# Performance work log

Hardware: AMD Instinct MI355X
Metric: run time of the kernel (lower is better)

The kernel has to match this reference:

```python
import jax, jax.numpy as jnp
import numpy as np
from jax import lax

B, C, H, W = 8, 64, 128, 128
K = 3  # deformable kernel size, padding=1, stride=1


def conv3x3(x, w, b=None):
    # x: [B,Cin,H,W], w: [Cout,Cin,3,3]
    y = lax.conv_general_dilated(x, w, (1, 1), 'SAME',
                                 dimension_numbers=('NCHW', 'OIHW', 'NCHW'))
    if b is not None:
        y = y + b[None, :, None, None]
    return y


def leaky_relu(x, slope=0.1):
    return jnp.where(x >= 0, x, slope * x)


def _bilinear_sample_one(feat, ys, xs):
    # feat: [C,H,W]; ys, xs: [KK,H,W] fractional sample coords (zero outside borders)
    h, w = feat.shape[1], feat.shape[2]
    y0 = jnp.floor(ys)
    x0 = jnp.floor(xs)
    wy = ys - y0  # [KK,H,W]
    wx = xs - x0

    def gather(yi, xi):
        valid = ((yi >= 0) & (yi < h) & (xi >= 0) & (xi < w)).astype(feat.dtype)
        yc = jnp.clip(yi, 0, h - 1).astype(jnp.int32)
        xc = jnp.clip(xi, 0, w - 1).astype(jnp.int32)
        v = feat[:, yc, xc]  # [C,KK,H,W]
        return v * valid[None]

    v00 = gather(y0, x0)
    v01 = gather(y0, x0 + 1)
    v10 = gather(y0 + 1, x0)
    v11 = gather(y0 + 1, x0 + 1)
    top = v00 * (1 - wx)[None] + v01 * wx[None]
    bot = v10 * (1 - wx)[None] + v11 * wx[None]
    return top * (1 - wy)[None] + bot * wy[None]  # [C,KK,H,W]


def deform_conv2d(x, offset, weight):
    # x: [B,Cin,H,W]; offset: [B,2*K*K,H,W] (torchvision order: per-tap (dy,dx));
    # weight: [Cout,Cin,K,K]; stride=1, pad=1, dilation=1, groups=1, no bias.
    b, cin, h, w = x.shape
    kk = K * K
    off = offset.reshape(b, kk, 2, h, w)
    dy, dx = off[:, :, 0], off[:, :, 1]  # [B,KK,H,W]
    hh = jnp.arange(h, dtype=x.dtype)[:, None]
    ww = jnp.arange(w, dtype=x.dtype)[None, :]
    ky = (jnp.arange(kk) // K - 1).astype(x.dtype)[None, :, None, None]
    kx = (jnp.arange(kk) % K - 1).astype(x.dtype)[None, :, None, None]
    ys = hh[None, None] + ky + dy  # [B,KK,H,W]
    xs = ww[None, None] + kx + dx
    sampled = jax.vmap(_bilinear_sample_one)(x, ys, xs)  # [B,Cin,KK,H,W]
    wflat = weight.reshape(weight.shape[0], cin, kk)
    return jnp.einsum('bckhw,ock->bohw', sampled, wflat)


def setup_inputs() -> dict:
    key = jax.random.key(0)
    ks = jax.random.split(key, 7)
    ref_feat = jax.random.normal(ks[0], (B, C, H, W), jnp.float32)
    target_feat = jax.random.normal(ks[1], (B, C, H, W), jnp.float32)
    w1 = jax.random.normal(ks[2], (C, 2 * C, 3, 3), jnp.float32) * 0.02
    b1 = jax.random.normal(ks[3], (C,), jnp.float32) * 0.02
    w2 = jax.random.normal(ks[4], (18, C, 3, 3), jnp.float32) * 0.02
    b2 = jax.random.normal(ks[5], (18,), jnp.float32) * 0.02
    wd = jax.random.normal(ks[6], (C, C, 3, 3), jnp.float32) * 0.05
    return {'ref_feat': ref_feat, 'target_feat': target_feat,
            'w1': w1, 'b1': b1, 'w2': w2, 'b2': b2, 'wd': wd}


def reference(ref_feat, target_feat, w1, b1, w2, b2, wd):
    concat_feat = jnp.concatenate([ref_feat, target_feat], axis=1)  # [B,2C,H,W]
    hmid = leaky_relu(conv3x3(concat_feat, w1, b1), 0.1)
    offset = conv3x3(hmid, w2, b2)  # [B,18,H,W]
    aligned_feat = deform_conv2d(target_feat, offset, wd)  # [B,C,H,W]
    return aligned_feat
```

## Files before the change

### kernel.cpp

```cpp
#include <hip/hip_runtime.h>
#include <hip/hip_fp16.h>

#define HW 128
#define PLANE (HW * HW)
#define OSTR 22

typedef __attribute__((ext_vector_type(8))) _Float16 f16x8;
typedef __attribute__((ext_vector_type(4))) float f32x4;

__device__ __forceinline__ unsigned short f2h(float f) {
  return __half_as_ushort(__float2half(f));
}

__device__ __forceinline__ void tile_from_bid_512(int bid, int& b, int& by, int& bx) {
  int wg = (bid & 7) * 64 + (bid >> 3);
  b = wg >> 6;
  int t = wg & 63;
  by = (t >> 3) << 4;
  bx = (t & 7) << 4;
}

__global__ __launch_bounds__(256) void pack_all_kernel(
    const float* __restrict__ w1, const float* __restrict__ w2,
    const float* __restrict__ wd, unsigned short* __restrict__ w1p,
    unsigned short* __restrict__ w2p, unsigned short* __restrict__ wdp) {
  int idx = blockIdx.x * 256 + threadIdx.x;
  if (idx < 73728) {
    int k = idx >> 6, n = idx & 63;
    int tap = k >> 7, ic = k & 127;
    w1p[((k >> 3) * 64 + n) * 8 + (k & 7)] = f2h(w1[(n * 128 + ic) * 9 + tap]);
  } else if (idx < 73728 + 18432) {
    int i = idx - 73728;
    int k = i >> 5, n = i & 31;
    int tap = k >> 6, ic = k & 63;
    float v = (n < 18) ? w2[(n * 64 + ic) * 9 + tap] : 0.f;
    w2p[((k >> 3) * 32 + n) * 8 + (k & 7)] = f2h(v);
  } else if (idx < 73728 + 18432 + 36864) {
    int i = idx - 73728 - 18432;
    int k = i >> 6, n = i & 63;
    int tap = k >> 6, ic = k & 63;
    wdp[((k >> 3) * 64 + n) * 8 + (k & 7)] = f2h(wd[(n * 64 + ic) * 9 + tap]);
  }
}

__global__ __launch_bounds__(256) void to_nhwc_kernel(
    const float* __restrict__ ref, const float* __restrict__ tgt,
    unsigned short* __restrict__ xref, unsigned short* __restrict__ xtgt) {
  __shared__ unsigned short lds[32][136];
  const int b = blockIdx.z, y = blockIdx.y, x0 = blockIdx.x * 32;
  for (int idx = threadIdx.x; idx < 4096; idx += 256) {
    int ic = idx >> 5, px = idx & 31;
    const float* src = (ic < 64) ? ref : tgt;
    lds[px][ic] = f2h(src[(b * 64 + (ic & 63)) * PLANE + y * HW + x0 + px]);
  }
  __syncthreads();
  for (int idx = threadIdx.x; idx < 512; idx += 256) {
    int px = idx >> 4, g = idx & 15;
    uint4 v = *(const uint4*)&lds[px][g * 8];
    size_t base = ((size_t)(b * HW + y) * HW + x0 + px) * 64;
    if (g < 8)
      *(uint4*)(xref + base + g * 8) = v;
    else
      *(uint4*)(xtgt + base + (g - 8) * 8) = v;
  }
}

__device__ __forceinline__ uint4 blend4(uint4 a, uint4 b, uint4 c, uint4 d,
                                        __half2 h00, __half2 h01, __half2 h10, __half2 h11) {
  union U { uint4 u; __half2 h[4]; };
  U A, B, C, D, R;
  A.u = a; B.u = b; C.u = c; D.u = d;
#pragma unroll
  for (int i = 0; i < 4; ++i)
    R.h[i] = __hfma2(D.h[i], h11, __hfma2(C.h[i], h10, __hfma2(B.h[i], h01, __hmul2(A.h[i], h00))));
  return R.u;
}

__global__ __launch_bounds__(512, 2) void mega_kernel(
    const unsigned short* __restrict__ xref, const unsigned short* __restrict__ xtgt,
    const unsigned short* __restrict__ w1p, const float* __restrict__ b1,
    const unsigned short* __restrict__ w2p, const float* __restrict__ b2,
    const unsigned short* __restrict__ wdp, float* __restrict__ out) {
  __shared__ __align__(16) unsigned short bufW[400 * 64];
  __shared__ __align__(8) float offsL[256 * OSTR];

  int b, by, bx;
  tile_from_bid_512(blockIdx.x, b, by, bx);
  const int tid = threadIdx.x, lane = tid & 63, w = tid >> 6;
  const int l15 = lane & 15, lg = lane >> 4;

  const unsigned short* rb = xref + (size_t)b * PLANE * 64;
  const unsigned short* tb = xtgt + (size_t)b * PLANE * 64;

  auto STAGE = [&](const unsigned short* src) {
    for (int i = tid; i < 3200; i += 512) {
      int rec = i >> 3, g = i & 7;
      int wy = rec / 20, wx = rec - wy * 20;
      int gy = by - 2 + wy, gx = bx - 2 + wx;
      uint4 v = make_uint4(0u, 0u, 0u, 0u);
      if ((unsigned)gy < 128u && (unsigned)gx < 128u)
        v = *(const uint4*)(src + ((size_t)gy * HW + gx) * 64 + g * 8);
      *(uint4*)(bufW + rec * 64 + ((g * 8) ^ ((rec & 7) << 3))) = v;
    }
  };

  int pyv[3], pxv[3];
#pragma unroll
  for (int n = 0; n < 3; ++n) {
    int p = (w * 3 + n) * 16 + l15;
    p = min(p, 323);
    pyv[n] = p / 18;
    pxv[n] = p - pyv[n] * 18;
  }

  f32x4 acc1[4][3];
#pragma unroll
  for (int mf = 0; mf < 4; ++mf)
#pragma unroll
    for (int n = 0; n < 3; ++n) acc1[mf][n] = (f32x4){0.f, 0.f, 0.f, 0.f};

  auto CONV1_HALF = [&](int c) {
#pragma unroll
    for (int tap = 0; tap < 9; ++tap) {
      const int ty = tap / 3, tx = tap - ty * 3;
#pragma unroll
      for (int ks = 0; ks < 2; ++ks) {
        f16x8 bp[3];
#pragma unroll
        for (int n = 0; n < 3; ++n) {
          int rec = (pyv[n] + ty) * 20 + pxv[n] + tx;
          bp[n] = *(const f16x8*)(bufW + rec * 64 + ((ks * 32 + lg * 8) ^ ((rec & 7) << 3)));
        }
        const int kb = tap * 16 + c * 8 + ks * 4 + lg;
        f16x8 aw[4];
#pragma unroll
        for (int mf = 0; mf < 4; ++mf)
          aw[mf] = *(const f16x8*)(w1p + (kb * 64 + mf * 16 + l15) * 8);
#pragma unroll
        for (int mf = 0; mf < 4; ++mf)
#pragma unroll
          for (int n = 0; n < 3; ++n)
            acc1[mf][n] = __builtin_amdgcn_mfma_f32_16x16x32_f16(aw[mf], bp[n], acc1[mf][n], 0, 0, 0);
      }
    }
  };

  STAGE(tb);
  __syncthreads();
  CONV1_HALF(1);
  __syncthreads();
  STAGE(rb);
  __syncthreads();
  CONV1_HALF(0);
  __syncthreads();

  unsigned short* hmidL = bufW;
#pragma unroll
  for (int mf = 0; mf < 4; ++mf) {
    const float4 bv = ((const float4*)b1)[mf * 4 + lg];
#pragma unroll
    for (int n = 0; n < 3; ++n) {
      const int p = (w * 3 + n) * 16 + l15;
      const bool valid = ((unsigned)(by - 1 + pyv[n]) < 128u) &&
                         ((unsigned)(bx - 1 + pxv[n]) < 128u);
      const float m = valid ? 1.f : 0.f;
      float v0 = acc1[mf][n][0] + bv.x;
      float v1 = acc1[mf][n][1] + bv.y;
      float v2 = acc1[mf][n][2] + bv.z;
      float v3 = acc1[mf][n][3] + bv.w;
      v0 = ((v0 >= 0.f) ? v0 : 0.1f * v0) * m;
      v1 = ((v1 >= 0.f) ? v1 : 0.1f * v1) * m;
      v2 = ((v2 >= 0.f) ? v2 : 0.1f * v2) * m;
      v3 = ((v3 >= 0.f) ? v3 : 0.1f * v3) * m;
      ushort4 s;
      s.x = f2h(v0); s.y = f2h(v1); s.z = f2h(v2); s.w = f2h(v3);
      *(ushort4*)(hmidL + p * 64 + ((mf * 16 + lg * 4) ^ ((p & 7) << 3))) = s;
    }
  }
  __syncthreads();

  f32x4 acc2[2][2];
#pragma unroll
  for (int q = 0; q < 2; ++q)
#pragma unroll
    for (int nf = 0; nf < 2; ++nf) acc2[q][nf] = (f32x4){0.f, 0.f, 0.f, 0.f};

#pragma unroll
  for (int tap = 0; tap < 9; ++tap) {
    const int ty = tap / 3, tx = tap - ty * 3;
#pragma unroll
    for (int ks = 0; ks < 2; ++ks) {
      f16x8 ap[2];
#pragma unroll
      for (int q = 0; q < 2; ++q) {
        int p = (w * 2 + q + ty) * 18 + l15 + tx;
        ap[q] = *(const f16x8*)(hmidL + p * 64 + ((ks * 32 + lg * 8) ^ ((p & 7) << 3)));
      }
      const int kb = tap * 8 + ks * 4 + lg;
      f16x8 bw[2];
#pragma unroll
      for (int nf = 0; nf < 2; ++nf)
        bw[nf] = *(const f16x8*)(w2p + (kb * 32 + nf * 16 + l15) * 8);
#pragma unroll
      for (int q = 0; q < 2; ++q)
#pragma unroll
        for (int nf = 0; nf < 2; ++nf)
          acc2[q][nf] = __builtin_amdgcn_mfma_f32_16x16x32_f16(ap[q], bw[nf], acc2[q][nf], 0, 0, 0);
    }
  }
#pragma unroll
  for (int nf = 0; nf < 2; ++nf) {
    const int oc = nf * 16 + l15;
    if (oc < 18) {
      const float bias = b2[oc];
#pragma unroll
      for (int q = 0; q < 2; ++q)
#pragma unroll
        for (int reg = 0; reg < 4; ++reg) {
          int px = (w * 2 + q) * 16 + lg * 4 + reg;
          offsL[px * OSTR + oc] = acc2[q][nf][reg] + bias;
        }
    }
  }
  __syncthreads();

  STAGE(tb);
  __syncthreads();

  f32x4 acc[2][4];
#pragma unroll
  for (int q = 0; q < 2; ++q)
#pragma unroll
    for (int nf = 0; nf < 4; ++nf) acc[q][nf] = (f32x4){0.f, 0.f, 0.f, 0.f};

  const int x = bx + l15;

  for (int kk = 0; kk < 9; ++kk) {
    const int kdy = kk / 3 - 1, kdx = kk - (kk / 3) * 3 - 1;
    f16x8 af[2][2];
#pragma unroll
    for (int q = 0; q < 2; ++q) {
      const int y = by + w * 2 + q;
      const int px_lin = (w * 2 + q) * 16 + l15;
      const float2 o2 = *(const float2*)(&offsL[px_lin * OSTR + kk * 2]);
      float ys = (float)(y + kdy) + o2.x;
      float xs = (float)(x + kdx) + o2.y;
      float y0f = floorf(ys), x0f = floorf(xs);
      float wy = ys - y0f, wx = xs - x0f;
      int y0 = (int)y0f, x0i = (int)x0f;
      int y1 = y0 + 1, x1 = x0i + 1;
      float vy0 = (y0 >= 0 && y0 < HW) ? 1.f : 0.f;
      float vy1 = (y1 >= 0 && y1 < HW) ? 1.f : 0.f;
      float vx0 = (x0i >= 0 && x0i < HW) ? 1.f : 0.f;
      float vx1 = (x1 >= 0 && x1 < HW) ? 1.f : 0.f;
      int y0c = min(max(y0, 0), HW - 1), y1c = min(max(y1, 0), HW - 1);
      int x0c = min(max(x0i, 0), HW - 1), x1c = min(max(x1, 0), HW - 1);
      __half2 h00 = __float2half2_rn((1.f - wy) * (1.f - wx) * vy0 * vx0);
      __half2 h01 = __float2half2_rn((1.f - wy) * wx * vy0 * vx1);
      __half2 h10 = __float2half2_rn(wy * (1.f - wx) * vy1 * vx0);
      __half2 h11 = __float2half2_rn(wy * wx * vy1 * vx1);

      const int wy0 = y0c - by + 2, wy1 = y1c - by + 2;
      const int wx0 = x0c - bx + 2, wx1 = x1c - bx + 2;
      const bool inw = ((unsigned)wy0 < 20u) && ((unsigned)wy1 < 20u) &&
                       ((unsigned)wx0 < 20u) && ((unsigned)wx1 < 20u);
      const int r00 = wy0 * 20 + wx0, r01 = wy0 * 20 + wx1;
      const int r10 = wy1 * 20 + wx0, r11 = wy1 * 20 + wx1;
      const unsigned short* p00 = tb + (y0c * HW + x0c) * 64 + lg * 8;
      const unsigned short* p01 = tb + (y0c * HW + x1c) * 64 + lg * 8;
      const unsigned short* p10 = tb + (y1c * HW + x0c) * 64 + lg * 8;
      const unsigned short* p11 = tb + (y1c * HW + x1c) * 64 + lg * 8;
#pragma unroll
      for (int ks = 0; ks < 2; ++ks) {
        uint4 c0, c1, c2, c3;
        const int ko = ks * 32 + lg * 8;
        if (inw) {
          c0 = *(const uint4*)(bufW + r00 * 64 + (ko ^ ((r00 & 7) << 3)));
          c1 = *(const uint4*)(bufW + r01 * 64 + (ko ^ ((r01 & 7) << 3)));
          c2 = *(const uint4*)(bufW + r10 * 64 + (ko ^ ((r10 & 7) << 3)));
          c3 = *(const uint4*)(bufW + r11 * 64 + (ko ^ ((r11 & 7) << 3)));
        } else {
          c0 = *(const uint4*)(p00 + ks * 32);
          c1 = *(const uint4*)(p01 + ks * 32);
          c2 = *(const uint4*)(p10 + ks * 32);
          c3 = *(const uint4*)(p11 + ks * 32);
        }
        uint4 r = blend4(c0, c1, c2, c3, h00, h01, h10, h11);
        af[q][ks] = *(const f16x8*)&r;
      }
    }

#pragma unroll
    for (int ks = 0; ks < 2; ++ks) {
      const int kb = kk * 8 + ks * 4 + lg;
      f16x8 bw[4];
#pragma unroll
      for (int nf = 0; nf < 4; ++nf)
        bw[nf] = *(const f16x8*)(wdp + (kb * 64 + nf * 16 + l15) * 8);
#pragma unroll
      for (int q = 0; q < 2; ++q)
#pragma unroll
        for (int nf = 0; nf < 4; ++nf)
          acc[q][nf] = __builtin_amdgcn_mfma_f32_16x16x32_f16(af[q][ks], bw[nf], acc[q][nf], 0, 0, 0);
    }
  }

  const int px0 = bx + lg * 4;
#pragma unroll
  for (int q = 0; q < 2; ++q) {
    const int py = by + w * 2 + q;
#pragma unroll
    for (int nf = 0; nf < 4; ++nf) {
      const int oc = nf * 16 + l15;
      float4 o;
      o.x = acc[q][nf][0];
      o.y = acc[q][nf][1];
      o.z = acc[q][nf][2];
      o.w = acc[q][nf][3];
      *(float4*)(out + (size_t)(b * 64 + oc) * PLANE + py * HW + px0) = o;
    }
  }
}

extern "C" void kernel_launch(void* const* d_in, const int* in_sizes, int n_in,
                              void* d_out, int out_size, void* d_ws, size_t ws_size,
                              hipStream_t stream) {
  const float* ref = (const float*)d_in[0];
  const float* tgt = (const float*)d_in[1];
  const float* w1  = (const float*)d_in[2];
  const float* b1  = (const float*)d_in[3];
  const float* w2  = (const float*)d_in[4];
  const float* b2  = (const float*)d_in[5];
  const float* wd  = (const float*)d_in[6];
  float* out = (float*)d_out;

  char* ws = (char*)d_ws;
  unsigned short* xref = (unsigned short*)ws;
  unsigned short* xtgt = (unsigned short*)(ws + 16777216);
  unsigned short* w1p  = (unsigned short*)(ws + 33554432);
  unsigned short* w2p  = (unsigned short*)(ws + 33701888);
  unsigned short* wdp  = (unsigned short*)(ws + 33738752);

  pack_all_kernel<<<504, 256, 0, stream>>>(w1, w2, wd, w1p, w2p, wdp);

  to_nhwc_kernel<<<dim3(4, 128, 8), 256, 0, stream>>>(ref, tgt, xref, xtgt);

  mega_kernel<<<512, 512, 0, stream>>>(xref, xtgt, w1p, b1, w2p, b2, wdp, out);
}
```

Baseline: 108.2 us.

## Read conv1 inputs directly from global memory and pad LDS rows instead of swizzling

The first convolution no longer stages the reference and target tiles into shared memory. Each lane loads its B-operand fragments straight from global memory with bounds checks, which also removes the staging barriers around conv1. The shared-memory buffer switches from an XOR-swizzled 64-element row layout to a padded 72-element stride, and the hmid and deform-sampling accesses are updated to match. This trades LDS staging and synchronisation for repeated global/L1 loads across the nine taps, and enlarges the shared-memory footprint, which may limit occupancy.

```diff
diff --git a/kernel.cpp b/kernel.cpp
--- a/kernel.cpp
+++ b/kernel.cpp
@@ -3,6 +3,7 @@
 
 #define HW 128
 #define PLANE (HW * HW)
+#define WSTR 72
 #define OSTR 22
 
 typedef __attribute__((ext_vector_type(8))) _Float16 f16x8;
@@ -81,7 +82,7 @@
     const unsigned short* __restrict__ w1p, const float* __restrict__ b1,
     const unsigned short* __restrict__ w2p, const float* __restrict__ b2,
     const unsigned short* __restrict__ wdp, float* __restrict__ out) {
-  __shared__ __align__(16) unsigned short bufW[400 * 64];
+  __shared__ __align__(16) unsigned short bufW[400 * WSTR];
   __shared__ __align__(8) float offsL[256 * OSTR];
 
   int b, by, bx;
@@ -100,7 +101,7 @@
       uint4 v = make_uint4(0u, 0u, 0u, 0u);
       if ((unsigned)gy < 128u && (unsigned)gx < 128u)
         v = *(const uint4*)(src + ((size_t)gy * HW + gx) * 64 + g * 8);
-      *(uint4*)(bufW + rec * 64 + ((g * 8) ^ ((rec & 7) << 3))) = v;
+      *(uint4*)(bufW + rec * WSTR + g * 8) = v;
     }
   };
 
@@ -119,7 +120,7 @@
 #pragma unroll
     for (int n = 0; n < 3; ++n) acc1[mf][n] = (f32x4){0.f, 0.f, 0.f, 0.f};
 
-  auto CONV1_HALF = [&](int c) {
+  auto CONV1_HALF = [&](int c, const unsigned short* src) {
 #pragma unroll
     for (int tap = 0; tap < 9; ++tap) {
       const int ty = tap / 3, tx = tap - ty * 3;
@@ -128,8 +129,12 @@
         f16x8 bp[3];
 #pragma unroll
         for (int n = 0; n < 3; ++n) {
-          int rec = (pyv[n] + ty) * 20 + pxv[n] + tx;
-          bp[n] = *(const f16x8*)(bufW + rec * 64 + ((ks * 32 + lg * 8) ^ ((rec & 7) << 3)));
+          const int gy = by + pyv[n] + ty - 2;
+          const int gx = bx + pxv[n] + tx - 2;
+          uint4 v = make_uint4(0u, 0u, 0u, 0u);
+          if ((unsigned)gy < 128u && (unsigned)gx < 128u)
+            v = *(const uint4*)(src + ((size_t)gy * HW + gx) * 64 + ks * 32 + lg * 8);
+          bp[n] = *(const f16x8*)&v;
         }
         const int kb = tap * 16 + c * 8 + ks * 4 + lg;
         f16x8 aw[4];
@@ -145,14 +150,8 @@
     }
   };
 
-  STAGE(tb);
-  __syncthreads();
-  CONV1_HALF(1);
-  __syncthreads();
-  STAGE(rb);
-  __syncthreads();
-  CONV1_HALF(0);
-  __syncthreads();
+  CONV1_HALF(0, rb);
+  CONV1_HALF(1, tb);
 
   unsigned short* hmidL = bufW;
 #pragma unroll
@@ -174,7 +173,7 @@
       v3 = ((v3 >= 0.f) ? v3 : 0.1f * v3) * m;
       ushort4 s;
       s.x = f2h(v0); s.y = f2h(v1); s.z = f2h(v2); s.w = f2h(v3);
-      *(ushort4*)(hmidL + p * 64 + ((mf * 16 + lg * 4) ^ ((p & 7) << 3))) = s;
+      *(ushort4*)(hmidL + p * WSTR + mf * 16 + lg * 4) = s;
     }
   }
   __syncthreads();
@@ -194,7 +193,7 @@
 #pragma unroll
       for (int q = 0; q < 2; ++q) {
         int p = (w * 2 + q + ty) * 18 + l15 + tx;
-        ap[q] = *(const f16x8*)(hmidL + p * 64 + ((ks * 32 + lg * 8) ^ ((p & 7) << 3)));
+        ap[q] = *(const f16x8*)(hmidL + p * WSTR + ks * 32 + lg * 8);
       }
       const int kb = tap * 8 + ks * 4 + lg;
       f16x8 bw[2];
@@ -275,10 +274,10 @@
         uint4 c0, c1, c2, c3;
         const int ko = ks * 32 + lg * 8;
         if (inw) {
-          c0 = *(const uint4*)(bufW + r00 * 64 + (ko ^ ((r00 & 7) << 3)));
-          c1 = *(const uint4*)(bufW + r01 * 64 + (ko ^ ((r01 & 7) << 3)));
-          c2 = *(const uint4*)(bufW + r10 * 64 + (ko ^ ((r10 & 7) << 3)));
-          c3 = *(const uint4*)(bufW + r11 * 64 + (ko ^ ((r11 & 7) << 3)));
+          c0 = *(const uint4*)(bufW + r00 * WSTR + ko);
+          c1 = *(const uint4*)(bufW + r01 * WSTR + ko);
+          c2 = *(const uint4*)(bufW + r10 * WSTR + ko);
+          c3 = *(const uint4*)(bufW + r11 * WSTR + ko);
         } else {
           c0 = *(const uint4*)(p00 + ks * 32);
           c1 = *(const uint4*)(p01 + ks * 32);
```

Result: slower. 131.3 us (+21.4%).
